# Optimization experiments

Hardware: AMD Instinct MI355X
Metric: run time of the kernel (lower is better)

The kernel has to match this reference:

```python
import jax, jax.numpy as jnp
import numpy as np
from jax.scipy.special import logsumexp
from jax.scipy.linalg import solve_triangular

STATE_DIM = 64
OBS_DIM = 32
NUM_PARTICLES = 32768
T = 64
DT = 0.01
DAMPING = 0.99
TEMPERATURE = 0.5
LOG_2PI = float(np.log(2.0 * np.pi))


def setup_inputs() -> dict:
    key = jax.random.key(0)
    ks = jax.random.split(key, 6)
    observations = jax.random.normal(ks[0], (T + 1, OBS_DIM), dtype=jnp.float32)
    A = 0.1 * jax.random.normal(ks[1], (STATE_DIM, STATE_DIM), dtype=jnp.float32)
    C = 0.1 * jax.random.normal(ks[2], (OBS_DIM, STATE_DIM), dtype=jnp.float32)
    Q_terms = 0.01 * jax.random.normal(ks[3], (STATE_DIM, STATE_DIM, STATE_DIM), dtype=jnp.float32)
    # torch init: eye * 0.1; add small perturbation so gradients are non-trivial
    Q_chol = 0.1 * jnp.eye(STATE_DIM, dtype=jnp.float32) + 0.005 * jax.random.normal(ks[4], (STATE_DIM, STATE_DIM), dtype=jnp.float32)
    R_chol = 0.1 * jnp.eye(OBS_DIM, dtype=jnp.float32) + 0.005 * jax.random.normal(ks[5], (OBS_DIM, OBS_DIM), dtype=jnp.float32)
    return {"observations": observations, "A": A, "C": C, "Q_terms": Q_terms,
            "Q_chol": Q_chol, "R_chol": R_chol}


def _obs_log_prob(particles, obs, C, L_R):
    """MVN log p(obs | C @ x, R) for each particle. particles [N,D], obs [obs_dim]."""
    mean = particles @ C.T                       # [N, obs_dim]
    diff = obs[None, :] - mean                   # [N, obs_dim]
    z = solve_triangular(L_R, diff.T, lower=True)  # [obs_dim, N]
    log_det_half = jnp.sum(jnp.log(jnp.diag(L_R)))
    return -0.5 * (OBS_DIM * LOG_2PI + jnp.sum(z * z, axis=0)) - log_det_half


def _smc_forward(observations, A, C, Q_terms, Q_chol, R_chol):
    R = R_chol @ R_chol.T
    L_R = jnp.linalg.cholesky(R)

    key = jax.random.key(42)
    k_init, k_scan = jax.random.split(key)
    particles = jax.random.normal(k_init, (NUM_PARTICLES, STATE_DIM), dtype=jnp.float32)
    log_weights = _obs_log_prob(particles, observations[0], C, L_R)

    def step(carry, xs):
        particles, log_weights, lml = carry
        obs_t, t = xs
        k = jax.random.fold_in(k_scan, t)
        k1, k2 = jax.random.split(k)

        log_w = log_weights - logsumexp(log_weights)
        u = jax.random.uniform(k1, (NUM_PARTICLES,), dtype=jnp.float32)
        gumbel = -jnp.log(-jnp.log(u + 1e-10) + 1e-10)
        ancestor_probs = jax.nn.softmax((log_w + gumbel) / TEMPERATURE)
        # Faithful to torch broadcast: collapses to the weighted-mean particle [1, D]
        resampled = (ancestor_probs @ particles)[None, :]

        noise = jax.random.normal(k2, (NUM_PARTICLES, STATE_DIM), dtype=jnp.float32) @ Q_chol.T
        quad = jnp.einsum('ijk,bj,bk->bi', Q_terms, resampled, resampled)  # [1, D]
        mean = resampled + DT * (resampled @ A.T + quad) * DAMPING          # [1, D]
        new_particles = mean + noise                                        # [N, D]

        new_log_weights = _obs_log_prob(new_particles, obs_t, C, L_R)
        new_lml = lml + logsumexp(new_log_weights)
        return (new_particles, new_log_weights, new_lml), None

    init = (particles, log_weights, jnp.zeros((), dtype=jnp.float32))
    (_, _, lml), _ = jax.lax.scan(step, init, (observations[1:], jnp.arange(T)))
    return lml[None]  # shape (1,) like torch


def reference(observations, A, C, Q_terms, Q_chol, R_chol):
    return _smc_forward(observations, A, C, Q_terms, Q_chol, R_chol)
```

## Files before the change

### kernel.cpp

```cpp
#include <hip/hip_runtime.h>
#include <cstdint>

#define NPART 32768
#define HALFN 16384

#define WS_W     0
#define WS_M     2048
#define WS_B     4096
#define WS_C0    6176
#define WS_KI    6178
#define WS_NK    6180
#define WS_UK    6308
#define WS_P4    6440
#define WS_PSE   8488
#define WS_QP64  24872
#define WS_END   25384

#define ATS32(p, v) __hip_atomic_store((p), (v), __ATOMIC_RELAXED, __HIP_MEMORY_SCOPE_AGENT)
#define ATL32(p)    __hip_atomic_load((p), __ATOMIC_RELAXED, __HIP_MEMORY_SCOPE_AGENT)
#define ATS64(p, v) __hip_atomic_store((p), (v), __ATOMIC_RELAXED, __HIP_MEMORY_SCOPE_AGENT)
#define ATL64(p)    __hip_atomic_load((p), __ATOMIC_RELAXED, __HIP_MEMORY_SCOPE_AGENT)

struct HK { uint32_t a, b; };

__host__ __device__ inline HK tf2x32(uint32_t k0, uint32_t k1, uint32_t x0, uint32_t x1) {
  uint32_t kx = k0 ^ k1 ^ 0x1BD11BDAu;
#define TF_R(r) { x0 += x1; x1 = (x1 << (r)) | (x1 >> (32 - (r))); x1 ^= x0; }
  x0 += k0; x1 += k1;
  TF_R(13) TF_R(15) TF_R(26) TF_R(6)
  x0 += k1; x1 += kx + 1u;
  TF_R(17) TF_R(29) TF_R(16) TF_R(24)
  x0 += kx; x1 += k0 + 2u;
  TF_R(13) TF_R(15) TF_R(26) TF_R(6)
  x0 += k0; x1 += k1 + 3u;
  TF_R(17) TF_R(29) TF_R(16) TF_R(24)
  x0 += k1; x1 += kx + 4u;
  TF_R(13) TF_R(15) TF_R(26) TF_R(6)
  x0 += kx; x1 += k0 + 5u;
#undef TF_R
  HK r; r.a = x0; r.b = x1; return r;
}

__device__ inline float erfinv_f(float x) {
  float w = -log1pf(-x * x);
  float p;
  if (w < 5.0f) {
    w -= 2.5f;
    p = 2.81022636e-08f;
    p = fmaf(p, w, 3.43273939e-07f);
    p = fmaf(p, w, -3.5233877e-06f);
    p = fmaf(p, w, -4.39150654e-06f);
    p = fmaf(p, w, 0.00021858087f);
    p = fmaf(p, w, -0.00125372503f);
    p = fmaf(p, w, -0.00417768164f);
    p = fmaf(p, w, 0.246640727f);
    p = fmaf(p, w, 1.50140941f);
  } else {
    w = sqrtf(w) - 3.0f;
    p = -0.000200214257f;
    p = fmaf(p, w, 0.000100950558f);
    p = fmaf(p, w, 0.00134934322f);
    p = fmaf(p, w, -0.00367342844f);
    p = fmaf(p, w, 0.00573950773f);
    p = fmaf(p, w, -0.0076224613f);
    p = fmaf(p, w, 0.00943887047f);
    p = fmaf(p, w, 1.00167406f);
    p = fmaf(p, w, 2.83297682f);
  }
  return p * x;
}

__device__ inline float u01(uint32_t bits) {
  return __uint_as_float((bits >> 9) | 0x3f800000u) - 1.0f;
}

__device__ inline uint64_t packfs(float v, uint32_t sq) {
  return ((uint64_t)sq << 32) | (uint64_t)__float_as_uint(v);
}

__global__ __launch_bounds__(1024) void kp_kernel(float* __restrict__ ws,
    const float* __restrict__ obs, const float* __restrict__ Cm,
    const float* __restrict__ Qc, const float* __restrict__ Rc) {
  __shared__ float Ls[32][32];
  __shared__ float Li[32][32];
  __shared__ float Wsh[32][64];
  const int tid = threadIdx.x;
  const int i = tid >> 5, j = tid & 31;
  uint32_t* wsu = (uint32_t*)ws;
  for (int idx = WS_P4 + tid; idx < WS_END; idx += 1024) wsu[idx] = 0u;
  if (tid <= 64) {
    HK p0 = tf2x32(0u, 42u, 0u, 2u);
    HK p1 = tf2x32(0u, 42u, 1u, 3u);
    uint32_t ks0 = p0.b, ks1 = p1.b;
    HK f = tf2x32(ks0, ks1, 0u, (uint32_t)tid);
    HK q0 = tf2x32(f.a, f.b, 0u, 2u);
    HK q1 = tf2x32(f.a, f.b, 1u, 3u);
    wsu[WS_UK + 2 * tid] = q0.a; wsu[WS_UK + 2 * tid + 1] = q1.a;
    if (tid < 64) { wsu[WS_NK + 2 * tid] = q0.b; wsu[WS_NK + 2 * tid + 1] = q1.b; }
    if (tid == 0) { wsu[WS_KI] = p0.a; wsu[WS_KI + 1] = p1.a; }
  }
  {
    float a = 0.0f;
    for (int k = 0; k < 32; ++k) a = fmaf(Rc[i * 32 + k], Rc[j * 32 + k], a);
    Ls[i][j] = a;
  }
  __syncthreads();
  for (int k = 0; k < 32; ++k) {
    if (tid == 0) Ls[k][k] = sqrtf(Ls[k][k]);
    __syncthreads();
    if (tid > k && tid < 32) Ls[tid][k] /= Ls[k][k];
    __syncthreads();
    if (i > k && j > k && j <= i) Ls[i][j] = fmaf(-Ls[i][k], Ls[j][k], Ls[i][j]);
    __syncthreads();
  }
  if (tid < 32) {
    for (int r = 0; r < 32; ++r) Li[r][tid] = 0.0f;
    Li[tid][tid] = 1.0f / Ls[tid][tid];
    for (int r = tid + 1; r < 32; ++r) {
      float s = 0.0f;
      for (int m = tid; m < r; ++m) s = fmaf(Ls[r][m], Li[m][tid], s);
      Li[r][tid] = -s / Ls[r][r];
    }
  }
  __syncthreads();
  if (tid == 0) {
    float ld = 0.0f;
    for (int k = 0; k < 32; ++k) ld += logf(Ls[k][k]);
    ws[WS_C0] = -0.5f * 32.0f * 1.8378770664093453f - ld;
  }
  for (int idx = tid; idx < 2048; idx += 1024) {
    int o = idx >> 6, d = idx & 63;
    float a = 0.0f;
    for (int k = 0; k < 32; ++k) a = fmaf(Li[o][k], Cm[k * 64 + d], a);
    Wsh[o][d] = a;
    ws[WS_W + idx] = a;
  }
  __syncthreads();
  for (int idx = tid; idx < 2048; idx += 1024) {
    int o = idx >> 6, d = idx & 63;
    float a = 0.0f;
    for (int k = 0; k < 64; ++k) a = fmaf(Wsh[o][k], Qc[k * 64 + d], a);
    ws[WS_M + idx] = a;
  }
  for (int idx = tid; idx < 2080; idx += 1024) {
    int t = idx >> 5, o = idx & 31;
    float a = 0.0f;
    for (int k = 0; k < 32; ++k) a = fmaf(Li[o][k], obs[t * 32 + k], a);
    ws[WS_B + idx] = a;
  }
}

__global__ __launch_bounds__(512, 2) void kmain_kernel(
    float* __restrict__ ws, const float* __restrict__ Am,
    const float* __restrict__ Qcg, const float* __restrict__ Qt,
    float* __restrict__ dout) {
  __shared__ __align__(16) float Ms[2048];
  __shared__ __align__(16) float Wm[2048];
  __shared__ __align__(16) float As[4096];
  __shared__ __align__(16) float Qcs[4096];
  __shared__ __align__(16) float Qs[1024];
  __shared__ float hC[32];
  __shared__ float rS[64], uS[64], mnS[64];
  __shared__ float ebL[256];
  __shared__ float redA[256], redB[256], redC[256], redD[256];
  __shared__ float SEw[8][64];
  __shared__ float wred[8][4];
  __shared__ float sc[8];
  __shared__ uint32_t keyL[260];

  const int tid = threadIdx.x;
  const int bid = blockIdx.x;
  uint32_t* wsu = (uint32_t*)ws;
  uint64_t* qp64 = (uint64_t*)(ws + WS_QP64);

  for (int i = tid; i < 2048; i += 512) { Ms[i] = ws[WS_M + i]; Wm[i] = ws[WS_W + i]; }
  for (int i = tid; i < 4096; i += 512) { As[i] = Am[i]; Qcs[i] = Qcg[i]; }
  {
    const int i0 = (bid >> 2) * 4096 + (bid & 3) * 1024;
    for (int i = tid; i < 1024; i += 512) Qs[i] = Qt[i0 + i];
  }
  for (int i = tid; i < 128; i += 512) keyL[i] = wsu[WS_NK + i];
  for (int i = tid; i < 130; i += 512) keyL[128 + i] = wsu[WS_UK + i];
  if (tid == 0) { keyL[258] = wsu[WS_KI]; keyL[259] = wsu[WS_KI + 1]; sc[4] = 0.0f; }
  if (tid < 32) hC[tid] = ws[WS_B + tid];
  const float C0 = ws[WS_C0];
  __syncthreads();

  const int pr = tid >> 3;
  const int l8 = tid & 7;
  const int p = bid * 64 + pr;
  const int d0 = l8 * 8;
  const int wv = tid >> 6, ln = tid & 63;

  float Elo[8], Ehi[8], gl, gh;
  float aL[4], aH[4];

  auto poll64 = [&](uint64_t* pp, uint32_t sq) -> float {
    uint64_t q;
    for (;;) {
      q = ATL64(pp);
      if ((uint32_t)(q >> 32) >= sq) break;
      __builtin_amdgcn_s_sleep(1);
    }
    return __uint_as_float((uint32_t)q);
  };

  auto genE8 = [&](uint32_t k0, uint32_t k1) {
    const uint32_t fb = (uint32_t)(p * 64 + d0);
#pragma unroll
    for (int j = 0; j < 8; ++j) {
      HK o = tf2x32(k0, k1, fb + (uint32_t)j, fb + (uint32_t)j + 1048576u);
      float fl = u01(o.a), fh = u01(o.b);
      float ul = fmaxf(-0.99999994f, fmaf(fl, 2.0f, -0.99999994f));
      float uh = fmaxf(-0.99999994f, fmaf(fh, 2.0f, -0.99999994f));
      Elo[j] = 1.41421354f * erfinv_f(ul);
      Ehi[j] = 1.41421354f * erfinv_f(uh);
    }
  };
  auto genG = [&](uint32_t k0, uint32_t k1) {
    HK og = tf2x32(k0, k1, (uint32_t)p, (uint32_t)(p + 16384));
    gl = -logf(-logf(u01(og.a) + 1e-10f) + 1e-10f);
    gh = -logf(-logf(u01(og.b) + 1e-10f) + 1e-10f);
  };

  auto ringME = [&](const float* matL) {
#pragma unroll
    for (int q = 0; q < 4; ++q) { aL[q] = 0.f; aH[q] = 0.f; }
#pragma unroll
    for (int k = 0; k < 8; ++k) {
      if (k) {
#pragma unroll
        for (int q = 0; q < 4; ++q) {
          aL[q] = __shfl(aL[q], (l8 + 1) & 7, 8);
          aH[q] = __shfl(aH[q], (l8 + 1) & 7, 8);
        }
      }
      const int ow = ((l8 + k) & 7) * 4;
#pragma unroll
      for (int q = 0; q < 4; ++q) {
        const float* mr = matL + (ow + q) * 64 + d0;
        float4 m0 = *(const float4*)mr;
        float4 m1 = *(const float4*)(mr + 4);
        float t0 = aL[q];
        t0 = fmaf(m0.x, Elo[0], t0); t0 = fmaf(m0.y, Elo[1], t0);
        t0 = fmaf(m0.z, Elo[2], t0); t0 = fmaf(m0.w, Elo[3], t0);
        t0 = fmaf(m1.x, Elo[4], t0); t0 = fmaf(m1.y, Elo[5], t0);
        t0 = fmaf(m1.z, Elo[6], t0); t0 = fmaf(m1.w, Elo[7], t0);
        aL[q] = t0;
        float t1 = aH[q];
        t1 = fmaf(m0.x, Ehi[0], t1); t1 = fmaf(m0.y, Ehi[1], t1);
        t1 = fmaf(m0.z, Ehi[2], t1); t1 = fmaf(m0.w, Ehi[3], t1);
        t1 = fmaf(m1.x, Ehi[4], t1); t1 = fmaf(m1.y, Ehi[5], t1);
        t1 = fmaf(m1.z, Ehi[6], t1); t1 = fmaf(m1.w, Ehi[7], t1);
        aH[q] = t1;
      }
    }
  };

  auto tailStore = [&](uint32_t sq) {
    const int ob = ((l8 + 7) & 7) * 4;
    float s2l = 0.f, s2h = 0.f;
#pragma unroll
    for (int q = 0; q < 4; ++q) {
      float zl = hC[ob + q] - aL[q], zh = hC[ob + q] - aH[q];
      s2l = fmaf(zl, zl, s2l); s2h = fmaf(zh, zh, s2h);
    }
#pragma unroll
    for (int m = 1; m < 8; m <<= 1) { s2l += __shfl_xor(s2l, m, 8); s2h += __shfl_xor(s2h, m, 8); }
    const float lwL = C0 - 0.5f * s2l, lwH = C0 - 0.5f * s2h;
    const float yl = (lwL + gl) * 2.0f, yh = (lwH + gh) * 2.0f;
    float mv = fmaxf(yl, yh), ml = fmaxf(lwL, lwH);
#pragma unroll
    for (int m = 1; m < 64; m <<= 1) {
      mv = fmaxf(mv, __shfl_xor(mv, m, 64));
      ml = fmaxf(ml, __shfl_xor(ml, m, 64));
    }
    if (ln == 0) { wred[wv][0] = mv; wred[wv][1] = ml; }
    __syncthreads();
    if (tid == 0) {
      float a = wred[0][0], b = wred[0][1];
      for (int q = 1; q < 8; ++q) { a = fmaxf(a, wred[q][0]); b = fmaxf(b, wred[q][1]); }
      sc[0] = a; sc[1] = b;
    }
    __syncthreads();
    const float myb = sc[0], mlb = sc[1];
    const float wLo = expf(yl - myb), wHi = expf(yh - myb);
    float vzy = (l8 == 0) ? (wLo + wHi) : 0.0f;
    float vzl = (l8 == 0) ? (expf(lwL - mlb) + expf(lwH - mlb)) : 0.0f;
#pragma unroll
    for (int m = 1; m < 64; m <<= 1) { vzy += __shfl_xor(vzy, m, 64); vzl += __shfl_xor(vzl, m, 64); }
    if (ln == 0) { wred[wv][2] = vzy; wred[wv][3] = vzl; }
    float v[8];
#pragma unroll
    for (int j = 0; j < 8; ++j) v[j] = fmaf(wHi, Ehi[j], wLo * Elo[j]);
#pragma unroll
    for (int m = 8; m < 64; m <<= 1) {
#pragma unroll
      for (int j = 0; j < 8; ++j) v[j] += __shfl_xor(v[j], m, 64);
    }
    if (ln < 8) {
#pragma unroll
      for (int j = 0; j < 8; ++j) SEw[wv][ln * 8 + j] = v[j];
    }
    __syncthreads();
    float zl2 = 0.0f;
    if (tid < 64) {
      float ssum = SEw[0][tid];
      for (int q = 1; q < 8; ++q) ssum += SEw[q][tid];
      ATS32(ws + WS_PSE + (bid << 6) + tid, ssum);
    }
    if (tid == 0) {
      float zy = wred[0][2];
      zl2 = wred[0][3];
      for (int q = 1; q < 8; ++q) { zy += wred[q][2]; zl2 += wred[q][3]; }
      float* pb = ws + WS_P4 + (bid << 3);
      ATS32(pb + 0, sc[0]);
      ATS32(pb + 1, sc[1]);
      ATS32(pb + 2, zy);
    }
    if (tid < 64) asm volatile("s_waitcnt vmcnt(0)" ::: "memory");
    if (tid == 0)
      ATS64((uint64_t*)(ws + WS_P4 + (bid << 3) + 4), packfs(zl2, sq));
  };

  auto combine = [&](int s) {
    const uint32_t sq = (uint32_t)(s + 1);
    if (tid < 256) {
      float* pb = ws + WS_P4 + (tid << 3);
      float zl = poll64((uint64_t*)(pb + 4), sq);
      asm volatile("" ::: "memory");
      redA[tid] = ATL32(pb + 0);
      redB[tid] = ATL32(pb + 1);
      redC[tid] = ATL32(pb + 2);
      redD[tid] = zl;
    }
    __syncthreads();
    float pse[32];
    const int d = tid & 63, c = tid >> 6;
#pragma unroll
    for (int b8 = 0; b8 < 32; ++b8)
      pse[b8] = ATL32(ws + WS_PSE + (((c << 5) + b8) << 6) + d);
    if (tid < 64) {
      const int l = tid;
      float a0 = redA[l], a1 = redA[l + 64], a2 = redA[l + 128], a3 = redA[l + 192];
      float b0 = redB[l], b1 = redB[l + 64], b2 = redB[l + 128], b3 = redB[l + 192];
      float myg = fmaxf(fmaxf(a0, a2), fmaxf(a1, a3));
      float mlg = fmaxf(fmaxf(b0, b2), fmaxf(b1, b3));
#pragma unroll
      for (int m = 32; m >= 1; m >>= 1) {
        myg = fmaxf(myg, __shfl_xor(myg, m, 64));
        mlg = fmaxf(mlg, __shfl_xor(mlg, m, 64));
      }
      myg = __shfl(myg, 0, 64); mlg = __shfl(mlg, 0, 64);
      float zy0 = redC[l], zy1 = redC[l + 64], zy2 = redC[l + 128], zy3 = redC[l + 192];
      float zl0 = redD[l], zl1 = redD[l + 64], zl2 = redD[l + 128], zl3 = redD[l + 192];
      float e0 = expf(a0 - myg), e1 = expf(a1 - myg), e2 = expf(a2 - myg), e3 = expf(a3 - myg);
      ebL[l] = e0; ebL[l + 64] = e1; ebL[l + 128] = e2; ebL[l + 192] = e3;
      float zyS = (e0 * zy0 + e2 * zy2) + (e1 * zy1 + e3 * zy3);
      float f0 = expf(b0 - mlg) * zl0, f1 = expf(b1 - mlg) * zl1;
      float f2 = expf(b2 - mlg) * zl2, f3 = expf(b3 - mlg) * zl3;
      float zlS = (f0 + f2) + (f1 + f3);
#pragma unroll
      for (int m = 32; m >= 1; m >>= 1) {
        zyS += __shfl_xor(zyS, m, 64);
        zlS += __shfl_xor(zlS, m, 64);
      }
      if (l == 0) {
        sc[2] = zyS;
        if (s > 0) sc[4] += mlg + logf(zlS);
      }
    }
    __syncthreads();
    const float Zy = sc[2];
    {
      float pp = 0.0f;
#pragma unroll
      for (int b8 = 0; b8 < 32; ++b8)
        pp = fmaf(ebL[(c << 5) + b8], pse[b8], pp);
      SEw[c][d] = pp;
    }
    __syncthreads();
    if (tid < 64) {
      float sg = SEw[0][tid];
      for (int cc = 1; cc < 8; ++cc) sg += SEw[cc][tid];
      uS[tid] = sg / Zy;
    }
    __syncthreads();
    if (tid < 64) {
      float r;
      if (s == 0) r = uS[tid];
      else {
        r = mnS[tid];
        const float* qr = Qcs + tid * 64;
        for (int k2 = 0; k2 < 64; ++k2) r = fmaf(uS[k2], qr[k2], r);
      }
      rS[tid] = r;
    }
    __syncthreads();
  };

  auto quadPub = [&](int s) {
    const uint32_t sq = (uint32_t)(s + 1);
    if (tid < 256) {
      const int jl = tid >> 4, kc = tid & 15;
      const float* qr = Qs + jl * 64 + kc * 4;
      float t0 = qr[0] * rS[kc * 4];
      t0 = fmaf(qr[1], rS[kc * 4 + 1], t0);
      t0 = fmaf(qr[2], rS[kc * 4 + 2], t0);
      t0 = fmaf(qr[3], rS[kc * 4 + 3], t0);
      redA[tid] = t0 * rS[(bid & 3) * 16 + jl];
    }
    __syncthreads();
    if (tid < 64) {
      float q0 = redA[tid], q1 = redA[tid + 64], q2 = redA[tid + 128], q3 = redA[tid + 192];
      float qs = (q0 + q2) + (q1 + q3);
#pragma unroll
      for (int m = 32; m >= 1; m >>= 1) qs += __shfl_xor(qs, m, 64);
      if (tid == 0) ATS64(qp64 + bid, packfs(qs, sq));
    }
  };

  auto meanH = [&](int s) {
    const uint32_t sq = (uint32_t)(s + 1);
    if (tid < 64) {
      float ar = 0.0f;
      const float* arow = As + tid * 64;
      for (int k2 = 0; k2 < 64; ++k2) ar = fmaf(arow[k2], rS[k2], ar);
      uint64_t* qb = qp64 + (tid << 2);
      uint64_t u0, u1, u2, u3;
      for (;;) {
        u0 = ATL64(qb + 0); u1 = ATL64(qb + 1);
        u2 = ATL64(qb + 2); u3 = ATL64(qb + 3);
        bool ok = ((uint32_t)(u0 >> 32) >= sq) && ((uint32_t)(u1 >> 32) >= sq) &&
                  ((uint32_t)(u2 >> 32) >= sq) && ((uint32_t)(u3 >> 32) >= sq);
        if (__all(ok)) break;
        __builtin_amdgcn_s_sleep(1);
      }
      float qd = __uint_as_float((uint32_t)u0) + __uint_as_float((uint32_t)u1) +
                 __uint_as_float((uint32_t)u2) + __uint_as_float((uint32_t)u3);
      mnS[tid] = rS[tid] + 0.0099f * (ar + qd);
    }
    __syncthreads();
    asm volatile("" ::: "memory");
    if (tid < 32) {
      float hv = ws[WS_B + (s + 1) * 32 + tid];
      const float* wrow = Wm + tid * 64;
      for (int d2 = 0; d2 < 64; ++d2) hv = fmaf(-wrow[d2], mnS[d2], hv);
      hC[tid] = hv;
    }
    __syncthreads();
  };

  genE8(keyL[258], keyL[259]);
  genG(keyL[128], keyL[129]);
  ringME(Wm);
  tailStore(1u);

  for (int s = 0; s < 64; ++s) {
    genE8(keyL[2 * s], keyL[2 * s + 1]);
    genG(keyL[128 + 2 * (s + 1)], keyL[128 + 2 * (s + 1) + 1]);
    ringME(Ms);
    combine(s);
    quadPub(s);
    meanH(s);
    tailStore((uint32_t)(s + 2));
  }

  if (bid == 0) {
    const uint32_t sq = 65u;
    float pml = 0.f, pzlv = 0.f;
    if (tid < 256) {
      float* pb = ws + WS_P4 + (tid << 3);
      pzlv = poll64((uint64_t*)(pb + 4), sq);
      asm volatile("" ::: "memory");
      pml = ATL32(pb + 1);
      redB[tid] = pml;
    }
    __syncthreads();
    for (int st = 128; st > 0; st >>= 1) {
      if (tid < st) redB[tid] = fmaxf(redB[tid], redB[tid + st]);
      __syncthreads();
    }
    const float mlwg = redB[0];
    __syncthreads();
    if (tid < 256) redB[tid] = expf(pml - mlwg) * pzlv;
    __syncthreads();
    for (int st = 128; st > 0; st >>= 1) {
      if (tid < st) redB[tid] += redB[tid + st];
      __syncthreads();
    }
    if (tid == 0) dout[0] = sc[4] + mlwg + logf(redB[0]);
  }
}

extern "C" void kernel_launch(void* const* d_in, const int* in_sizes, int n_in,
                              void* d_out, int out_size, void* d_ws, size_t ws_size,
                              hipStream_t stream) {
  const float* obs = (const float*)d_in[0];
  const float* Am = (const float*)d_in[1];
  const float* Cm = (const float*)d_in[2];
  const float* Qt = (const float*)d_in[3];
  const float* Qc = (const float*)d_in[4];
  const float* Rc = (const float*)d_in[5];
  float* ws = (float*)d_ws;
  float* out = (float*)d_out;
  (void)in_sizes; (void)n_in; (void)out_size; (void)ws_size;

  kp_kernel<<<dim3(1), dim3(1024), 0, stream>>>(ws, obs, Cm, Qc, Rc);

  void* params[] = { (void*)&ws, (void*)&Am, (void*)&Qc, (void*)&Qt, (void*)&out };
  hipLaunchCooperativeKernel((const void*)kmain_kernel, dim3(256), dim3(512),
                             params, 0, stream);
}
```

Measured before the change: 1.230 ms.

## Tag every published partial with a sequence number and reorder per-step stages

Per-block partial results (maxima, sums, projected state sums) are now published as 64-bit value/sequence pairs, so readers poll each value directly. This replaces the store-then-vmcnt-fence-then-flag pattern and the separate flag poll. The step loop is reordered so combine and quadPub run first, and noise generation for the next step is moved after tailStore so it can overlap other blocks' publishing. The cost is doubled workspace traffic for the per-dimension partials and a wider polling loop over 32 values per thread.

```diff
diff --git a/kernel.cpp b/kernel.cpp
--- a/kernel.cpp
+++ b/kernel.cpp
@@ -12,9 +12,9 @@
 #define WS_NK    6180
 #define WS_UK    6308
 #define WS_P4    6440
-#define WS_PSE   8488
-#define WS_QP64  24872
-#define WS_END   25384
+#define WS_PSE64 8488
+#define WS_QP64  41256
+#define WS_END   41768
 
 #define ATS32(p, v) __hip_atomic_store((p), (v), __ATOMIC_RELAXED, __HIP_MEMORY_SCOPE_AGENT)
 #define ATL32(p)    __hip_atomic_load((p), __ATOMIC_RELAXED, __HIP_MEMORY_SCOPE_AGENT)
@@ -171,6 +171,8 @@
   const int tid = threadIdx.x;
   const int bid = blockIdx.x;
   uint32_t* wsu = (uint32_t*)ws;
+  uint64_t* p4 = (uint64_t*)(ws + WS_P4);
+  uint64_t* pse64 = (uint64_t*)(ws + WS_PSE64);
   uint64_t* qp64 = (uint64_t*)(ws + WS_QP64);
 
   for (int i = tid; i < 2048; i += 512) { Ms[i] = ws[WS_M + i]; Wm[i] = ws[WS_W + i]; }
@@ -303,43 +305,60 @@
       for (int j = 0; j < 8; ++j) SEw[wv][ln * 8 + j] = v[j];
     }
     __syncthreads();
-    float zl2 = 0.0f;
     if (tid < 64) {
       float ssum = SEw[0][tid];
       for (int q = 1; q < 8; ++q) ssum += SEw[q][tid];
-      ATS32(ws + WS_PSE + (bid << 6) + tid, ssum);
+      ATS64(pse64 + (bid << 6) + tid, packfs(ssum, sq));
     }
     if (tid == 0) {
       float zy = wred[0][2];
-      zl2 = wred[0][3];
+      float zl2 = wred[0][3];
       for (int q = 1; q < 8; ++q) { zy += wred[q][2]; zl2 += wred[q][3]; }
-      float* pb = ws + WS_P4 + (bid << 3);
-      ATS32(pb + 0, sc[0]);
-      ATS32(pb + 1, sc[1]);
-      ATS32(pb + 2, zy);
-    }
-    if (tid < 64) asm volatile("s_waitcnt vmcnt(0)" ::: "memory");
-    if (tid == 0)
-      ATS64((uint64_t*)(ws + WS_P4 + (bid << 3) + 4), packfs(zl2, sq));
+      uint64_t* bp = p4 + (bid << 2);
+      ATS64(bp + 0, packfs(myb, sq));
+      ATS64(bp + 1, packfs(mlb, sq));
+      ATS64(bp + 2, packfs(zy, sq));
+      ATS64(bp + 3, packfs(zl2, sq));
+    }
   };
 
   auto combine = [&](int s) {
     const uint32_t sq = (uint32_t)(s + 1);
     if (tid < 256) {
-      float* pb = ws + WS_P4 + (tid << 3);
-      float zl = poll64((uint64_t*)(pb + 4), sq);
-      asm volatile("" ::: "memory");
-      redA[tid] = ATL32(pb + 0);
-      redB[tid] = ATL32(pb + 1);
-      redC[tid] = ATL32(pb + 2);
-      redD[tid] = zl;
-    }
-    __syncthreads();
+      uint64_t* bp = p4 + (tid << 2);
+      uint64_t h0, h1, h2, h3;
+      for (;;) {
+        h0 = ATL64(bp + 0); h1 = ATL64(bp + 1);
+        h2 = ATL64(bp + 2); h3 = ATL64(bp + 3);
+        bool ok = ((uint32_t)(h0 >> 32) >= sq) && ((uint32_t)(h1 >> 32) >= sq) &&
+                  ((uint32_t)(h2 >> 32) >= sq) && ((uint32_t)(h3 >> 32) >= sq);
+        if (__all(ok)) break;
+        __builtin_amdgcn_s_sleep(1);
+      }
+      redA[tid] = __uint_as_float((uint32_t)h0);
+      redB[tid] = __uint_as_float((uint32_t)h1);
+      redC[tid] = __uint_as_float((uint32_t)h2);
+      redD[tid] = __uint_as_float((uint32_t)h3);
+    }
     float pse[32];
-    const int d = tid & 63, c = tid >> 6;
-#pragma unroll
-    for (int b8 = 0; b8 < 32; ++b8)
-      pse[b8] = ATL32(ws + WS_PSE + (((c << 5) + b8) << 6) + d);
+    {
+      const int d = tid & 63, c = tid >> 6;
+      uint64_t v[32];
+      for (;;) {
+#pragma unroll
+        for (int b8 = 0; b8 < 32; ++b8)
+          v[b8] = ATL64(pse64 + ((((c << 5) + b8) << 6) + d));
+        bool ok = true;
+#pragma unroll
+        for (int b8 = 0; b8 < 32; ++b8)
+          ok = ok && ((uint32_t)(v[b8] >> 32) >= sq);
+        if (__all(ok)) break;
+        __builtin_amdgcn_s_sleep(1);
+      }
+#pragma unroll
+      for (int b8 = 0; b8 < 32; ++b8) pse[b8] = __uint_as_float((uint32_t)v[b8]);
+    }
+    __syncthreads();
     if (tid < 64) {
       const int l = tid;
       float a0 = redA[l], a1 = redA[l + 64], a2 = redA[l + 128], a3 = redA[l + 192];
@@ -373,6 +392,7 @@
     __syncthreads();
     const float Zy = sc[2];
     {
+      const int d = tid & 63, c = tid >> 6;
       float pp = 0.0f;
 #pragma unroll
       for (int b8 = 0; b8 < 32; ++b8)
@@ -441,7 +461,6 @@
       mnS[tid] = rS[tid] + 0.0099f * (ar + qd);
     }
     __syncthreads();
-    asm volatile("" ::: "memory");
     if (tid < 32) {
       float hv = ws[WS_B + (s + 1) * 32 + tid];
       const float* wrow = Wm + tid * 64;
@@ -455,25 +474,26 @@
   genG(keyL[128], keyL[129]);
   ringME(Wm);
   tailStore(1u);
+  genE8(keyL[0], keyL[1]);
 
   for (int s = 0; s < 64; ++s) {
-    genE8(keyL[2 * s], keyL[2 * s + 1]);
+    combine(s);
+    quadPub(s);
     genG(keyL[128 + 2 * (s + 1)], keyL[128 + 2 * (s + 1) + 1]);
     ringME(Ms);
-    combine(s);
-    quadPub(s);
     meanH(s);
     tailStore((uint32_t)(s + 2));
+    if (s < 63)
+      genE8(keyL[2 * (s + 1)], keyL[2 * (s + 1) + 1]);
   }
 
   if (bid == 0) {
     const uint32_t sq = 65u;
     float pml = 0.f, pzlv = 0.f;
     if (tid < 256) {
-      float* pb = ws + WS_P4 + (tid << 3);
-      pzlv = poll64((uint64_t*)(pb + 4), sq);
-      asm volatile("" ::: "memory");
-      pml = ATL32(pb + 1);
+      uint64_t* bp = p4 + (tid << 2);
+      pml = poll64(bp + 1, sq);
+      pzlv = poll64(bp + 3, sq);
       redB[tid] = pml;
     }
     __syncthreads();
```

After: 1.306 ms. +6.2%, slower.
